# Kernel optimization log

Hardware: AMD Instinct MI355X
Metric: run time of the kernel (lower is better)

Reference implementation:

```python
import math
import jax, jax.numpy as jnp
import numpy as np

N_FILT = 80
FILT_DIM = 251
FS = 16000
PAD = 125


def _mel_init(n_filt, fs):
    low_freq_mel = 80.0
    high_freq_mel = 2595.0 * np.log10(1 + fs / 2 / 700)
    mel_points = np.linspace(low_freq_mel, high_freq_mel, n_filt)
    f_cos = 700.0 * (10 ** (mel_points / 2595.0) - 1)
    b1 = np.roll(f_cos, 1)
    b2 = np.roll(f_cos, -1)
    b1[0] = 30.0
    b2[-1] = fs / 2 - 100.0
    return (b1 / fs).astype(np.float32), ((b2 - b1) / fs).astype(np.float32)


def setup_inputs() -> dict:
    key = jax.random.key(0)
    kx, = jax.random.split(key, 1)
    x = jax.random.normal(kx, (32, 1, 32000), dtype=jnp.float32)
    b1, band = _mel_init(N_FILT, FS)
    return {"x": x, "filt_b1": jnp.asarray(b1), "filt_band": jnp.asarray(band)}


def _make_filters(filt_b1, filt_band):
    fs = float(FS)
    N = FILT_DIM
    two_pi = 2.0 * math.pi
    # t_right = 1..(N-1)/2 in samples, length (N-1)//2 = 125
    t_right = jnp.linspace(1.0, (N - 1) / 2, (N - 1) // 2, dtype=jnp.float32)
    min_f = 50.0 / fs
    beg = jnp.abs(filt_b1) + min_f                      # [F]
    end = beg + jnp.abs(filt_band) + min_f              # [F]

    def low_pass(f):  # f: [F] normalized freq -> [F, N] sinc low-pass
        arg = two_pi * (f * fs)[:, None] * t_right[None, :]   # [F, 125]
        y_right = jnp.sin(arg) / arg
        ones = jnp.ones((f.shape[0], 1), dtype=jnp.float32)
        y = jnp.concatenate([y_right[:, ::-1], ones, y_right], axis=1)  # [F, 251]
        return 2.0 * f[:, None] * y

    band_pass = low_pass(end) - low_pass(beg)           # [F, N]
    band_pass = band_pass / jnp.max(band_pass, axis=1, keepdims=True)
    # window uses n = linspace(0, N, N) exactly as torch.linspace(0, N, steps=N)
    n = jnp.linspace(0.0, float(N), N, dtype=jnp.float32)
    window = 0.54 - 0.46 * jnp.cos(two_pi * n / N)
    return band_pass * window                            # [F, N]


def reference(x, filt_b1, filt_band):
    filters = _make_filters(filt_b1, filt_band)          # [N_filt, Filt_dim]
    kernel = filters[:, None, :]                         # [O=N_filt, I=1, K]
    out = jax.lax.conv_general_dilated(
        x, kernel,
        window_strides=(1,),
        padding=[(PAD, PAD)],
        dimension_numbers=("NCH", "OIH", "NCH"),
    )
    return out
```

## Files before the change

kernel.cpp:

```cpp
#include <hip/hip_runtime.h>
#include <hip/hip_bf16.h>

#define N_FILT   80
#define FILT_DIM 251
#define PAD      125
#define SEQ      32000
#define BATCH    32
#define TWO_PI_F 6.28318530717958647692f

typedef __attribute__((ext_vector_type(8))) short short8;
typedef __attribute__((ext_vector_type(4))) float floatx4;

__global__ void gen_filters(const float* __restrict__ b1p,
                            const float* __restrict__ bandp,
                            unsigned short* __restrict__ afrag) {
    const int f = blockIdx.x;
    const int i = threadIdx.x;

    const float min_f = 0.003125f;
    float b1   = fabsf(b1p[f]);
    float band = fabsf(bandp[f]);
    float beg  = b1 + min_f;
    float end  = beg + band + min_f;

    float bp = -1e30f;
    if (i < FILT_DIM) {
        int d = i - PAD;
        float lpe, lpb;
        if (d == 0) { lpe = 2.0f*end; lpb = 2.0f*beg; }
        else {
            float kf = (float)(d < 0 ? -d : d);
            float ae = (TWO_PI_F * (end * 16000.0f)) * kf;
            float ab = (TWO_PI_F * (beg * 16000.0f)) * kf;
            lpe = (2.0f*end) * (sinf(ae)/ae);
            lpb = (2.0f*beg) * (sinf(ab)/ab);
        }
        bp = lpe - lpb;
    }

    __shared__ float red[256];
    red[i] = bp;
    __syncthreads();
    for (int s = 128; s > 0; s >>= 1) {
        if (i < s) red[i] = fmaxf(red[i], red[i+s]);
        __syncthreads();
    }
    float mx = red[0];

    float val = 0.0f;
    if (i < FILT_DIM) {
        float n = (float)i * (251.0f/250.0f);
        float w = 0.54f - 0.46f*cosf((TWO_PI_F*n)/251.0f);
        val = (bp/mx) * w;
    }
    __hip_bfloat16 h = __float2bfloat16(val);
    const int ft = f >> 4, m = f & 15;
    const int ks = i >> 5, q = (i >> 3) & 3, j = i & 7;
    afrag[((((ft*8+ks)*4+q)*16) + m)*8 + j] = *reinterpret_cast<unsigned short*>(&h);
}

#define BLK_POS 640
#define NPAIR   20
#define XS_H    904

__global__ __launch_bounds__(256) void conv_mfma(
        const float* __restrict__ x,
        const unsigned short* __restrict__ afrag,
        float* __restrict__ out) {
    __shared__ __align__(16) unsigned short ash[80*256];
    __shared__ __align__(16) unsigned short xsh[8*XS_H];

    const int b   = blockIdx.y;
    const int t0  = blockIdx.x * BLK_POS;
    const int tid = threadIdx.x;
    const float* xb = x + (size_t)b * SEQ;

    {
        const int4* src = reinterpret_cast<const int4*>(afrag);
        int4*       dst = reinterpret_cast<int4*>(ash);
        for (int i = tid; i < (80*256)/8; i += 256) dst[i] = src[i];
    }
    for (int c = 0; c < 8; ++c) {
        unsigned short* cp = xsh + c*XS_H;
        for (int m = tid; m < XS_H; m += 256) {
            int g = t0 - PAD + m + c;
            float v = (g >= 0 && g < SEQ) ? xb[g] : 0.0f;
            __hip_bfloat16 h = __float2bfloat16(v);
            cp[m] = *reinterpret_cast<unsigned short*>(&h);
        }
    }
    __syncthreads();

    const int lane = tid & 63;
    const int w    = tid >> 6;
    const int n    = lane & 15;
    const int q    = lane >> 4;
    const int cc   = n & 7;
    const int bbase = cc*XS_H + 8*q + 8*(n>>3);

    for (int pp = w; pp < NPAIR; pp += 4) {
        const int off0 = 32*pp;
        short8 B0[8], B1[8];
        #pragma unroll
        for (int ks = 0; ks < 8; ++ks) {
            B0[ks] = *reinterpret_cast<const short8*>(xsh + bbase + off0 + 32*ks);
            B1[ks] = *reinterpret_cast<const short8*>(xsh + bbase + off0 + 16 + 32*ks);
        }
        #pragma unroll
        for (int ft = 0; ft < 5; ++ft) {
            floatx4 a0 = {0.f,0.f,0.f,0.f}, a1 = {0.f,0.f,0.f,0.f};
            #pragma unroll
            for (int ks = 0; ks < 8; ++ks) {
                short8 A = *reinterpret_cast<const short8*>(ash + ((ft*8+ks)*64 + lane)*8);
                a0 = __builtin_amdgcn_mfma_f32_16x16x32_bf16(A, B0[ks], a0, 0, 0, 0);
                a1 = __builtin_amdgcn_mfma_f32_16x16x32_bf16(A, B1[ks], a1, 0, 0, 0);
            }
            size_t obase = ((size_t)(b*N_FILT + ft*16 + 4*q))*SEQ + t0 + off0 + n;
            #pragma unroll
            for (int r = 0; r < 4; ++r) {
                out[obase + (size_t)r*SEQ]      = a0[r];
                out[obase + (size_t)r*SEQ + 16] = a1[r];
            }
        }
    }
}

extern "C" void kernel_launch(void* const* d_in, const int* in_sizes, int n_in,
                              void* d_out, int out_size, void* d_ws, size_t ws_size,
                              hipStream_t stream) {
    const float* x    = (const float*)d_in[0];
    const float* b1   = (const float*)d_in[1];
    const float* band = (const float*)d_in[2];
    unsigned short* afrag = (unsigned short*)d_ws;
    float* out = (float*)d_out;

    gen_filters<<<N_FILT, 256, 0, stream>>>(b1, band, afrag);

    dim3 grid(SEQ / BLK_POS, BATCH);
    conv_mfma<<<grid, 256, 0, stream>>>(x, afrag, out);
}
```

Before: 378.3 us.

## Keep filter fragments in registers and swap MFMA operands for vectorized stores

```diff
diff --git a/kernel.cpp b/kernel.cpp
--- a/kernel.cpp
+++ b/kernel.cpp
@@ -59,30 +59,38 @@
     afrag[((((ft*8+ks)*4+q)*16) + m)*8 + j] = *reinterpret_cast<unsigned short*>(&h);
 }
 
-#define BLK_POS 640
-#define NPAIR   20
-#define XS_H    904
+#define BLK_POS 1280
+#define NPT     (BLK_POS/16)
+#define PT_W    (NPT/4)
+#define XS_LEN  1528
+#define XS_H    1544
 
-__global__ __launch_bounds__(256) void conv_mfma(
+__global__ __launch_bounds__(256, 2) void conv_mfma(
         const float* __restrict__ x,
         const unsigned short* __restrict__ afrag,
         float* __restrict__ out) {
-    __shared__ __align__(16) unsigned short ash[80*256];
     __shared__ __align__(16) unsigned short xsh[8*XS_H];
 
-    const int b   = blockIdx.y;
-    const int t0  = blockIdx.x * BLK_POS;
-    const int tid = threadIdx.x;
+    const int b    = blockIdx.y;
+    const int t0   = blockIdx.x * BLK_POS;
+    const int tid  = threadIdx.x;
+    const int lane = tid & 63;
+    const int w    = tid >> 6;
+    const int n    = lane & 15;
+    const int q    = lane >> 4;
     const float* xb = x + (size_t)b * SEQ;
 
-    {
-        const int4* src = reinterpret_cast<const int4*>(afrag);
-        int4*       dst = reinterpret_cast<int4*>(ash);
-        for (int i = tid; i < (80*256)/8; i += 256) dst[i] = src[i];
-    }
+    short8 F[5][8];
+    #pragma unroll
+    for (int ft = 0; ft < 5; ++ft)
+        #pragma unroll
+        for (int ks = 0; ks < 8; ++ks)
+            F[ft][ks] = *reinterpret_cast<const short8*>(
+                afrag + ((((ft*8+ks)*4+q)*16) + n)*8);
+
     for (int c = 0; c < 8; ++c) {
         unsigned short* cp = xsh + c*XS_H;
-        for (int m = tid; m < XS_H; m += 256) {
+        for (int m = tid; m < XS_LEN; m += 256) {
             int g = t0 - PAD + m + c;
             float v = (g >= 0 && g < SEQ) ? xb[g] : 0.0f;
             __hip_bfloat16 h = __float2bfloat16(v);
@@ -91,36 +99,24 @@
     }
     __syncthreads();
 
-    const int lane = tid & 63;
-    const int w    = tid >> 6;
-    const int n    = lane & 15;
-    const int q    = lane >> 4;
-    const int cc   = n & 7;
-    const int bbase = cc*XS_H + 8*q + 8*(n>>3);
+    const int abase = (lane & 7)*XS_H + 8*((lane >> 3) & 1) + 8*q;
+    float* ob = out + ((size_t)b*N_FILT + n)*SEQ + t0 + 4*q;
 
-    for (int pp = w; pp < NPAIR; pp += 4) {
-        const int off0 = 32*pp;
-        short8 B0[8], B1[8];
+    for (int t = 0; t < PT_W; ++t) {
+        const int pt = w*PT_W + t;
+        short8 A[8];
         #pragma unroll
-        for (int ks = 0; ks < 8; ++ks) {
-            B0[ks] = *reinterpret_cast<const short8*>(xsh + bbase + off0 + 32*ks);
-            B1[ks] = *reinterpret_cast<const short8*>(xsh + bbase + off0 + 16 + 32*ks);
-        }
+        for (int ks = 0; ks < 8; ++ks)
+            A[ks] = *reinterpret_cast<const short8*>(
+                xsh + abase + pt*16 + 32*ks);
         #pragma unroll
         for (int ft = 0; ft < 5; ++ft) {
-            floatx4 a0 = {0.f,0.f,0.f,0.f}, a1 = {0.f,0.f,0.f,0.f};
+            floatx4 acc = {0.f, 0.f, 0.f, 0.f};
             #pragma unroll
-            for (int ks = 0; ks < 8; ++ks) {
-                short8 A = *reinterpret_cast<const short8*>(ash + ((ft*8+ks)*64 + lane)*8);
-                a0 = __builtin_amdgcn_mfma_f32_16x16x32_bf16(A, B0[ks], a0, 0, 0, 0);
-                a1 = __builtin_amdgcn_mfma_f32_16x16x32_bf16(A, B1[ks], a1, 0, 0, 0);
-            }
-            size_t obase = ((size_t)(b*N_FILT + ft*16 + 4*q))*SEQ + t0 + off0 + n;
-            #pragma unroll
-            for (int r = 0; r < 4; ++r) {
-                out[obase + (size_t)r*SEQ]      = a0[r];
-                out[obase + (size_t)r*SEQ + 16] = a1[r];
-            }
+            for (int ks = 0; ks < 8; ++ks)
+                acc = __builtin_amdgcn_mfma_f32_16x16x32_bf16(
+                          A[ks], F[ft][ks], acc, 0, 0, 0);
+            *reinterpret_cast<floatx4*>(ob + (size_t)(ft*16)*SEQ + pt*16) = acc;
         }
     }
 }
```

Result: faster. 368.4 us (-2.6%).
